# Performance work log

Measured on AMD Instinct MI355X. Metric: run time of the kernel, lower is better.

The kernel has to match this reference:

```python
import jax, jax.numpy as jnp
import numpy as np

B, C, H, W = 2, 192, 64, 64
HEADS, KS = 6, 7
HD = C // HEADS


def setup_inputs() -> dict:
    key = jax.random.key(0)
    ks = jax.random.split(key, 6)
    s = 0.02
    return {
        "x": jax.random.normal(ks[0], (B, C, H, W), jnp.float32),
        "W_qkv1": jax.random.normal(ks[1], (3 * C, C, 1, 1), jnp.float32) * s,
        "b_qkv1": jnp.zeros((3 * C,), jnp.float32),
        "W_qkv2": jax.random.normal(ks[2], (3 * C, 1, 3, 3), jnp.float32) * s,  # depthwise
        "b_qkv2": jnp.zeros((3 * C,), jnp.float32),
        "temperature": jnp.ones((HEADS, 1, 1, 1), jnp.float32),
        "rpb": jax.random.normal(ks[3], (HEADS, 2 * KS - 1, 2 * KS - 1), jnp.float32) * s,
        "W_proj": jax.random.normal(ks[4], (C, C, 1, 1), jnp.float32) * s,
        "b_proj": jnp.zeros((C,), jnp.float32),
    }


def _conv(x, w, b, pad, groups=1):
    y = jax.lax.conv_general_dilated(
        x, w, (1, 1), pad,
        dimension_numbers=("NCHW", "OIHW", "NCHW"),
        feature_group_count=groups)
    return y + b[None, :, None, None]


def _l2norm(t, eps=1e-12):
    n = jnp.sqrt(jnp.sum(t * t, axis=-1, keepdims=True))
    return t / jnp.maximum(n, eps)


def _nbr_idx(L, K):
    # NATTEN shifted-window neighborhood (dilation=1): window start clamped to image.
    start = jnp.clip(jnp.arange(L) - K // 2, 0, L - K)
    idx = start[:, None] + jnp.arange(K)[None, :]        # [L,K] absolute neighbor index
    rel = idx - jnp.arange(L)[:, None] + (K - 1)         # [L,K] rpb table index
    return idx, rel


def _forward(x, W_qkv1, b_qkv1, W_qkv2, b_qkv2, temperature, rpb, W_proj, b_proj):
    Bq, Cq, Hh, Ww = x.shape
    heads = rpb.shape[0]
    K = (rpb.shape[1] + 1) // 2
    hd = Cq // heads
    qkv = _conv(_conv(x, W_qkv1, b_qkv1, "VALID"), W_qkv2, b_qkv2, "SAME", groups=3 * Cq)
    qkv = qkv.reshape(Bq, 3, heads, hd, Hh, Ww).transpose(1, 0, 2, 4, 5, 3)  # [3,B,h,H,W,d]
    q, k, v = qkv[0], qkv[1], qkv[2]
    q = _l2norm(q)
    k = _l2norm(k)
    idx_i, rel_i = _nbr_idx(Hh, K)
    idx_j, rel_j = _nbr_idx(Ww, K)
    ii = idx_i[:, None, :, None]  # [H,1,K,1]
    jj = idx_j[None, :, None, :]  # [1,W,1,K] -> broadcast [H,W,K,K]
    k_nb = k[:, :, ii, jj, :]     # [B,h,H,W,K,K,d]
    attn = jnp.einsum("bhijd,bhijkld->bhijkl", q, k_nb)
    bias = rpb[:, rel_i[:, None, :, None], rel_j[None, :, None, :]]  # [h,H,W,K,K]
    attn = (attn + bias[None]) * temperature.reshape(1, heads, 1, 1, 1, 1)
    attn = jax.nn.softmax(attn.reshape(Bq, heads, Hh, Ww, K * K), axis=-1)
    v_nb = v[:, :, ii, jj, :].reshape(Bq, heads, Hh, Ww, K * K, hd)
    out = jnp.einsum("bhijk,bhijkd->bhijd", attn, v_nb)
    out = out.transpose(0, 1, 4, 2, 3).reshape(Bq, Cq, Hh, Ww)
    return _conv(out, W_proj, b_proj, "VALID")


def reference(x, W_qkv1, b_qkv1, W_qkv2, b_qkv2, temperature, rpb, W_proj, b_proj):
    return _forward(x, W_qkv1, b_qkv1, W_qkv2, b_qkv2, temperature, rpb, W_proj, b_proj)
```

## Files before the change

### kernel.cpp

```cpp
#include <hip/hip_runtime.h>
#include <math.h>

#define HW 4096

typedef __attribute__((ext_vector_type(8))) short short8;
typedef __attribute__((ext_vector_type(8))) _Float16 half8;
typedef __attribute__((ext_vector_type(4))) float floatx4;

__device__ inline float bflo(unsigned u) { return __uint_as_float(u << 16); }
__device__ inline float bfhi(unsigned u) { return __uint_as_float(u & 0xffff0000u); }
__device__ inline unsigned short f2bf(float x) {
    unsigned u = __float_as_uint(x);
    return (unsigned short)((u + 0x7fffu + ((u >> 16) & 1u)) >> 16);
}
__device__ inline unsigned f2bf2(float lo, float hi) {
    unsigned a = __float_as_uint(lo), b = __float_as_uint(hi);
    a = (a + 0x7fffu + ((a >> 16) & 1u)) >> 16;
    b = (b + 0x7fffu + ((b >> 16) & 1u)) & 0xffff0000u;
    return a | b;
}
__device__ inline unsigned short f2h(float x) {
    _Float16 h = (_Float16)x;
    return __builtin_bit_cast(unsigned short, h);
}

__device__ inline void stage_halo(unsigned short* raw, const unsigned short* pl,
                                  int t, int npx, int gi0, int gj0)
{
    if (t < npx) {
        int ri = t >> 4, rj = t & 15;
        int gi = gi0 + ri, gj = gj0 + rj;
        uint4 v0 = {0u,0u,0u,0u}, v1 = v0, v2 = v0, v3 = v0;
        if ((unsigned)gi < 64u && (unsigned)gj < 64u) {
            const uint4* src = (const uint4*)(pl + (((gi << 6) + gj) << 5));
            v0 = src[0]; v1 = src[1]; v2 = src[2]; v3 = src[3];
        }
        uint4* d = (uint4*)&raw[t * 32];
        d[0] = v0; d[1] = v1; d[2] = v2; d[3] = v3;
    }
}


__global__ __launch_bounds__(256) void k_gq(const float* __restrict__ x,
    const float* __restrict__ W1, const float* __restrict__ b1,
    unsigned short* __restrict__ qkv)
{
    __shared__ __align__(16) unsigned short As[64 * 200];
    __shared__ __align__(16) unsigned short Bs[64 * 200];
    const int t = threadIdx.x;
    const int m0 = blockIdx.x * 64;
    const int n0 = blockIdx.y * 64;
    const int w = t >> 6, lane = t & 63;
    const int b = m0 >> 12, px0 = m0 & 4095;
    {
        const float* xb = x + ((size_t)(b * 192) << 12) + px0 + lane;
        const int cb = w * 48;
        #pragma unroll
        for (int r4 = 0; r4 < 12; ++r4) {
            float v0 = xb[(size_t)(cb + r4 * 4 + 0) << 12];
            float v1 = xb[(size_t)(cb + r4 * 4 + 1) << 12];
            float v2 = xb[(size_t)(cb + r4 * 4 + 2) << 12];
            float v3 = xb[(size_t)(cb + r4 * 4 + 3) << 12];
            *(uint2*)&As[lane * 200 + cb + r4 * 4] =
                make_uint2(f2bf2(v0, v1), f2bf2(v2, v3));
        }
    }
    #pragma unroll
    for (int pass = 0; pass < 12; ++pass) {
        int idx = pass * 256 + t;
        int row = idx / 48, ch = idx - row * 48;
        float4 wv = *(const float4*)&W1[(size_t)(n0 + row) * 192 + ch * 4];
        *(uint2*)&Bs[row * 200 + ch * 4] =
            make_uint2(f2bf2(wv.x, wv.y), f2bf2(wv.z, wv.w));
    }
    __syncthreads();
    const int lm = lane & 15, lq = lane >> 4;
    floatx4 acc[4] = {};
    #pragma unroll
    for (int ks = 0; ks < 6; ++ks) {
        short8 bf = *(const short8*)&Bs[(w * 16 + lm) * 200 + ks * 32 + lq * 8];
        #pragma unroll
        for (int mt = 0; mt < 4; ++mt) {
            short8 af = *(const short8*)&As[(mt * 16 + lm) * 200 + ks * 32 + lq * 8];
            acc[mt] = __builtin_amdgcn_mfma_f32_16x16x32_bf16(af, bf, acc[mt], 0, 0, 0);
        }
    }
    __syncthreads();
    const float bias = b1[n0 + w * 16 + lm];
    #pragma unroll
    for (int mt = 0; mt < 4; ++mt)
        #pragma unroll
        for (int r = 0; r < 4; ++r)
            As[(mt * 16 + lq * 4 + r) * 72 + w * 16 + lm] = f2bf(acc[mt][r] + bias);
    __syncthreads();
    #pragma unroll
    for (int pass = 0; pass < 2; ++pass) {
        int idx = pass * 256 + t;
        int m = idx >> 3, n8 = idx & 7;
        uint4 val = *(const uint4*)&As[m * 72 + n8 * 8];
        int oc = n0 + n8 * 8;
        int g = oc >> 5, d = oc & 31;
        *(uint4*)&qkv[((((size_t)(b * 18 + g) << 12) + px0 + m) << 5) + d] = val;
    }
}

__global__ __launch_bounds__(256) void k_attn(const unsigned short* __restrict__ qkv,
    const float* __restrict__ W2, const float* __restrict__ b2,
    const float* __restrict__ temp, const float* __restrict__ rpb,
    unsigned short* __restrict__ attnO)
{
    __shared__ __align__(16) char lds[49088];
    unsigned short* Ks  = (unsigned short*)lds;
    unsigned short* Ps  = (unsigned short*)lds;
    unsigned short* raw = (unsigned short*)(lds + 16640);
    unsigned short* Vts = (unsigned short*)(lds + 29696);
    float* rpbs = (float*)(lds + 44544);
    float* dwW  = (float*)(lds + 45248);
    float* dwB  = (float*)(lds + 48704);

    const int t = threadIdx.x;
    const int head = blockIdx.y, b = blockIdx.z;
    const int ti = blockIdx.x >> 3, tj = blockIdx.x & 7;
    const int i0 = ti * 8, j0 = tj * 8;
    const int r0 = min(max(i0 - 3, 0), 50), c0 = min(max(j0 - 3, 0), 50);
    const unsigned short* qpl = qkv + ((size_t)(b * 18 + head) << 17);
    const unsigned short* kpl = qkv + ((size_t)(b * 18 + 6 + head) << 17);
    const unsigned short* vpl = qkv + ((size_t)(b * 18 + 12 + head) << 17);

    for (int idx = t; idx < 864; idx += 256) {
        int plane = idx / 288, rem = idx - plane * 288;
        dwW[idx] = W2[(plane * 192 + head * 32 + (rem & 31)) * 9 + (rem >> 5)];
    }
    if (t < 96) dwB[t] = b2[(t >> 5) * 192 + head * 32 + (t & 31)];
    if (t < 169) rpbs[t] = rpb[head * 169 + t];
    for (int idx = t; idx < 448; idx += 256) {
        int row = (idx * 2341) >> 15;
        int c = idx - row * 14;
        ((unsigned*)(Vts + row * 232))[98 + c] = 0u;
    }

    for (int h = 0; h < 2; ++h) {
        stage_halo(raw, kpl, t, 144, r0 - 1 + h * 7, c0 - 1);
        __syncthreads();
        for (int s = 0; s < 2; ++s) {
            int task = s * 256 + t;
            if (task < 392) {
                int px = task >> 2, oct = task & 3;
                int rl = (px * 2341) >> 15, cc = px - rl * 14;
                float a[8];
                #pragma unroll
                for (int e = 0; e < 8; ++e) a[e] = dwB[32 + oct * 8 + e];
                #pragma unroll
                for (int tap = 0; tap < 9; ++tap) {
                    uint4 u = *(const uint4*)&raw[((rl + tap / 3) * 16 + cc + tap % 3) * 32 + oct * 8];
                    const float* wt = &dwW[(9 + tap) * 32 + oct * 8];
                    unsigned uu[4] = {u.x, u.y, u.z, u.w};
                    #pragma unroll
                    for (int e = 0; e < 4; ++e) {
                        a[e * 2]     = fmaf(bflo(uu[e]), wt[e * 2],     a[e * 2]);
                        a[e * 2 + 1] = fmaf(bfhi(uu[e]), wt[e * 2 + 1], a[e * 2 + 1]);
                    }
                }
                float ss = 0.f;
                #pragma unroll
                for (int e = 0; e < 8; ++e) ss = fmaf(a[e], a[e], ss);
                ss += __shfl_xor(ss, 1);
                ss += __shfl_xor(ss, 2);
                float rinv = 1.0f / fmaxf(sqrtf(ss), 1e-12f);
                int pxk = (h * 7 + rl) * 14 + cc;
                uint4 p;
                p.x = f2bf2(a[0] * rinv, a[1] * rinv);
                p.y = f2bf2(a[2] * rinv, a[3] * rinv);
                p.z = f2bf2(a[4] * rinv, a[5] * rinv);
                p.w = f2bf2(a[6] * rinv, a[7] * rinv);
                *(uint4*)&Ks[pxk * 40 + oct * 8] = p;
            }
        }
        __syncthreads();
    }

    for (int h = 0; h < 2; ++h) {
        stage_halo(raw, vpl, t, 144, r0 - 1 + h * 7, c0 - 1);
        __syncthreads();
        for (int s = 0; s < 2; ++s) {
            int task = s * 256 + t;
            if (task < 392) {
                int px = task >> 2, oct = task & 3;
                int rl = (px * 2341) >> 15, cc = px - rl * 14;
                float a[8];
                #pragma unroll
                for (int e = 0; e < 8; ++e) a[e] = dwB[64 + oct * 8 + e];
                #pragma unroll
                for (int tap = 0; tap < 9; ++tap) {
                    uint4 u = *(const uint4*)&raw[((rl + tap / 3) * 16 + cc + tap % 3) * 32 + oct * 8];
                    const float* wt = &dwW[(18 + tap) * 32 + oct * 8];
                    unsigned uu[4] = {u.x, u.y, u.z, u.w};
                    #pragma unroll
                    for (int e = 0; e < 4; ++e) {
                        a[e * 2]     = fmaf(bflo(uu[e]), wt[e * 2],     a[e * 2]);
                        a[e * 2 + 1] = fmaf(bfhi(uu[e]), wt[e * 2 + 1], a[e * 2 + 1]);
                    }
                }
                int pxk = (h * 7 + rl) * 14 + cc;
                #pragma unroll
                for (int e = 0; e < 8; ++e)
                    Vts[(oct * 8 + e) * 232 + pxk] = f2h(a[e]);
            }
        }
        __syncthreads();
    }

    stage_halo(raw, qpl, t, 160, i0 - 1, c0 - 1);
    __syncthreads();
    const int w = t >> 6, lane = t & 63;
    const int lm = lane & 15, lq = lane >> 4;
    const int px = w * 16 + lm;
    const int i = i0 + (px >> 3), j = j0 + (px & 7);
    const int qrow = px >> 3, qcol = (px & 7) + (j0 - c0);
    float qf[8];
    #pragma unroll
    for (int e = 0; e < 8; ++e) qf[e] = dwB[lq * 8 + e];
    #pragma unroll
    for (int tap = 0; tap < 9; ++tap) {
        uint4 u = *(const uint4*)&raw[((qrow + tap / 3) * 16 + qcol + tap % 3) * 32 + lq * 8];
        const float* wt = &dwW[tap * 32 + lq * 8];
        unsigned uu[4] = {u.x, u.y, u.z, u.w};
        #pragma unroll
        for (int e = 0; e < 4; ++e) {
            qf[e * 2]     = fmaf(bflo(uu[e]), wt[e * 2],     qf[e * 2]);
            qf[e * 2 + 1] = fmaf(bfhi(uu[e]), wt[e * 2 + 1], qf[e * 2 + 1]);
        }
    }
    float qs = 0.f;
    #pragma unroll
    for (int e = 0; e < 8; ++e) qs = fmaf(qf[e], qf[e], qs);
    qs += __shfl_xor(qs, 16);
    qs += __shfl_xor(qs, 32);
    float qinv = 1.0f / fmaxf(sqrtf(qs), 1e-12f);
    short8 bq;
    #pragma unroll
    for (int e = 0; e < 8; ++e) bq[e] = (short)f2bf(qf[e] * qinv);
    __syncthreads();

    floatx4 acc[13];
    #pragma unroll
    for (int mt = 0; mt < 13; ++mt) {
        short8 ak = *(const short8*)&Ks[(mt * 16 + lm) * 40 + lq * 8];
        floatx4 z = {0.f, 0.f, 0.f, 0.f};
        acc[mt] = __builtin_amdgcn_mfma_f32_16x16x32_bf16(ak, bq, z, 0, 0, 0);
    }
    __syncthreads();

    const int si = min(max(i - 3, 0), 57), sj = min(max(j - 3, 0), 57);
    const int vloi = si - r0, vloj = sj - c0;
    const int oi = r0 - i + 6, oj = c0 - j + 6;
    const float th = temp[head];
    float mx = -1e30f;
    #pragma unroll
    for (int mt = 0; mt < 13; ++mt) {
        int nb0 = mt * 16 + lq * 4;
        int rh0 = (nb0 * 2341) >> 15;
        int ch0 = nb0 - rh0 * 14;
        #pragma unroll
        for (int r = 0; r < 4; ++r) {
            int ch = ch0 + r, rh = rh0;
            if (ch >= 14) { ch -= 14; rh += 1; }
            int bidx = (rh + oi) * 13 + (ch + oj);
            float bias = rpbs[max(0, min(168, bidx))];
            bool valid = ((unsigned)(rh - vloi) <= 6u) && ((unsigned)(ch - vloj) <= 6u);
            float s = (acc[mt][r] + bias) * th;
            s = valid ? s : -1e30f;
            acc[mt][r] = s;
            mx = fmaxf(mx, s);
        }
    }
    mx = fmaxf(mx, __shfl_xor(mx, 16));
    mx = fmaxf(mx, __shfl_xor(mx, 32));
    float ssum = 0.f;
    #pragma unroll
    for (int mt = 0; mt < 13; ++mt)
        #pragma unroll
        for (int r = 0; r < 4; ++r) {
            float e = __expf(acc[mt][r] - mx);
            acc[mt][r] = e;
            ssum += e;
        }
    ssum += __shfl_xor(ssum, 16);
    ssum += __shfl_xor(ssum, 32);
    const float rs = 1.0f / ssum;

    if (lane < 32) {
        uint4 z4 = {0u, 0u, 0u, 0u};
        *(uint4*)&Ps[(w * 16 + (lane >> 1)) * 232 + 208 + (lane & 1) * 8] = z4;
    }
    #pragma unroll
    for (int mt = 0; mt < 13; ++mt) {
        unsigned lo = (unsigned)f2h(acc[mt][0] * rs) | ((unsigned)f2h(acc[mt][1] * rs) << 16);
        unsigned hi = (unsigned)f2h(acc[mt][2] * rs) | ((unsigned)f2h(acc[mt][3] * rs) << 16);
        *(uint2*)&Ps[px * 232 + mt * 16 + lq * 4] = make_uint2(lo, hi);
    }
    __syncthreads();

    floatx4 oacc[2] = {};
    #pragma unroll
    for (int ks = 0; ks < 7; ++ks) {
        half8 ap = *(const half8*)&Ps[(w * 16 + lm) * 232 + ks * 32 + lq * 8];
        #pragma unroll
        for (int n2 = 0; n2 < 2; ++n2) {
            half8 bv = *(const half8*)&Vts[(n2 * 16 + lm) * 232 + ks * 32 + lq * 8];
            oacc[n2] = __builtin_amdgcn_mfma_f32_16x16x32_f16(ap, bv, oacc[n2], 0, 0, 0);
        }
    }
    #pragma unroll
    for (int n2 = 0; n2 < 2; ++n2)
        #pragma unroll
        for (int r = 0; r < 4; ++r) {
            int p2 = w * 16 + lq * 4 + r;
            int i2 = i0 + (p2 >> 3), j2 = j0 + (p2 & 7);
            attnO[((size_t)((b << 12) + (i2 << 6) + j2)) * 192 + head * 32 + n2 * 16 + lm]
                = f2bf(oacc[n2][r]);
        }
}

__global__ __launch_bounds__(256) void k_gp(const unsigned short* __restrict__ Ain,
    const float* __restrict__ Wp, const float* __restrict__ bp,
    float* __restrict__ out)
{
    __shared__ __align__(16) unsigned short As[64 * 200];
    __shared__ __align__(16) unsigned short Bs[64 * 200];
    const int t = threadIdx.x;
    const int m0 = blockIdx.x * 64;
    const int n0 = blockIdx.y * 64;
    #pragma unroll
    for (int pass = 0; pass < 6; ++pass) {
        int idx = pass * 256 + t;
        int m = idx / 24, c16 = idx % 24;
        *(uint4*)&As[m * 200 + c16 * 8] = *(const uint4*)&Ain[(size_t)(m0 + m) * 192 + c16 * 8];
    }
    #pragma unroll
    for (int pass = 0; pass < 12; ++pass) {
        int idx = pass * 256 + t;
        int row = idx / 48, ch = idx - row * 48;
        float4 wv = *(const float4*)&Wp[(size_t)(n0 + row) * 192 + ch * 4];
        *(uint2*)&Bs[row * 200 + ch * 4] =
            make_uint2(f2bf2(wv.x, wv.y), f2bf2(wv.z, wv.w));
    }
    __syncthreads();
    const int w = t >> 6, lane = t & 63;
    const int lm = lane & 15, lq = lane >> 4;
    floatx4 acc[4] = {};
    #pragma unroll
    for (int ks = 0; ks < 6; ++ks) {
        short8 bf = *(const short8*)&Bs[(w * 16 + lm) * 200 + ks * 32 + lq * 8];
        #pragma unroll
        for (int mt = 0; mt < 4; ++mt) {
            short8 af = *(const short8*)&As[(mt * 16 + lm) * 200 + ks * 32 + lq * 8];
            acc[mt] = __builtin_amdgcn_mfma_f32_16x16x32_bf16(af, bf, acc[mt], 0, 0, 0);
        }
    }
    __syncthreads();
    float* fs = (float*)As;
    const float bias = bp[n0 + w * 16 + lm];
    #pragma unroll
    for (int mt = 0; mt < 4; ++mt)
        #pragma unroll
        for (int r = 0; r < 4; ++r)
            fs[(w * 16 + lm) * 68 + mt * 16 + lq * 4 + r] = acc[mt][r] + bias;
    __syncthreads();
    const int b = m0 >> 12, px0 = m0 & 4095;
    #pragma unroll
    for (int pass = 0; pass < 4; ++pass) {
        int idx = pass * 256 + t;
        int n = idx >> 4, m4 = idx & 15;
        float4 val = *(const float4*)&fs[n * 68 + m4 * 4];
        *(float4*)&out[((size_t)(b * 192 + n0 + n) << 12) + px0 + m4 * 4] = val;
    }
}

extern "C" void kernel_launch(void* const* d_in, const int* in_sizes, int n_in,
                              void* d_out, int out_size, void* d_ws, size_t ws_size,
                              hipStream_t stream) {
    const float* x    = (const float*)d_in[0];
    const float* W1   = (const float*)d_in[1];
    const float* b1   = (const float*)d_in[2];
    const float* W2   = (const float*)d_in[3];
    const float* b2   = (const float*)d_in[4];
    const float* temp = (const float*)d_in[5];
    const float* rpb  = (const float*)d_in[6];
    const float* Wp   = (const float*)d_in[7];
    const float* bp   = (const float*)d_in[8];
    float* out = (float*)d_out;

    char* ws = (char*)d_ws;
    unsigned short* qkv1b = (unsigned short*)(ws);
    unsigned short* attnO = (unsigned short*)(ws + 9437184);

    k_gq  <<<dim3(128, 9), 256, 0, stream>>>(x, W1, b1, qkv1b);
    k_attn<<<dim3(64, 6, 2), 256, 0, stream>>>(qkv1b, W2, b2, temp, rpb, attnO);
    k_gp  <<<dim3(128, 3), 256, 0, stream>>>(attnO, Wp, bp, out);
}
```

Measured before the change: 115.7 us.

## Fuse three kernels into one persistent kernel with grid-wide barriers

Merges the QKV GEMM, neighborhood attention and projection GEMM kernels into a single persistent kernel of 512 blocks. The blocks loop over tiles and are separated by atomic-counter grid barriers. The goal is to remove kernel launch gaps and the tail effects between stages. In exchange it adds a memset, spin-wait barriers, and a dependence on all 512 blocks being co-resident (2 per CU at 51 KB of LDS), which could deadlock if occupancy is lower. The later stages also leave some blocks idle.

```diff
diff --git a/kernel.cpp b/kernel.cpp
--- a/kernel.cpp
+++ b/kernel.cpp
@@ -1,7 +1,5 @@
 #include <hip/hip_runtime.h>
 #include <math.h>
-
-#define HW 4096
 
 typedef __attribute__((ext_vector_type(8))) short short8;
 typedef __attribute__((ext_vector_type(8))) _Float16 half8;
@@ -24,8 +22,8 @@
     return __builtin_bit_cast(unsigned short, h);
 }
 
-__device__ inline void stage_halo(unsigned short* raw, const unsigned short* pl,
-                                  int t, int npx, int gi0, int gj0)
+__device__ __forceinline__ void stage_halo(unsigned short* raw, const unsigned short* pl,
+                                           int t, int npx, int gi0, int gj0)
 {
     if (t < npx) {
         int ri = t >> 4, rj = t & 15;
@@ -40,16 +38,29 @@
     }
 }
 
-
-__global__ __launch_bounds__(256) void k_gq(const float* __restrict__ x,
-    const float* __restrict__ W1, const float* __restrict__ b1,
-    unsigned short* __restrict__ qkv)
-{
-    __shared__ __align__(16) unsigned short As[64 * 200];
-    __shared__ __align__(16) unsigned short Bs[64 * 200];
+__device__ __forceinline__ void grid_barrier(unsigned* bar, unsigned target)
+{
+    __syncthreads();
+    if (threadIdx.x == 0) {
+        __threadfence();
+        __hip_atomic_fetch_add(bar, 1u, __ATOMIC_RELEASE, __HIP_MEMORY_SCOPE_AGENT);
+        while (__hip_atomic_load(bar, __ATOMIC_ACQUIRE, __HIP_MEMORY_SCOPE_AGENT) < target) {
+            __builtin_amdgcn_s_sleep(8);
+        }
+        __threadfence();
+    }
+    __syncthreads();
+}
+
+
+__device__ void gq_tile(char* smem, int tile, const float* x, const float* W1,
+                        const float* b1, unsigned short* qkv)
+{
+    unsigned short* As = (unsigned short*)smem;
+    unsigned short* Bs = (unsigned short*)(smem + 25600);
     const int t = threadIdx.x;
-    const int m0 = blockIdx.x * 64;
-    const int n0 = blockIdx.y * 64;
+    const int m0 = (tile & 127) * 64;
+    const int n0 = (tile >> 7) * 64;
     const int w = t >> 6, lane = t & 63;
     const int b = m0 >> 12, px0 = m0 & 4095;
     {
@@ -102,14 +113,14 @@
         int g = oc >> 5, d = oc & 31;
         *(uint4*)&qkv[((((size_t)(b * 18 + g) << 12) + px0 + m) << 5) + d] = val;
     }
-}
-
-__global__ __launch_bounds__(256) void k_attn(const unsigned short* __restrict__ qkv,
-    const float* __restrict__ W2, const float* __restrict__ b2,
-    const float* __restrict__ temp, const float* __restrict__ rpb,
-    unsigned short* __restrict__ attnO)
-{
-    __shared__ __align__(16) char lds[49088];
+    __syncthreads();
+}
+
+__device__ void attn_tile(char* smem, int tile, const unsigned short* qkv,
+    const float* W2, const float* b2, const float* temp, const float* rpb,
+    unsigned short* attnO)
+{
+    char* lds = smem;
     unsigned short* Ks  = (unsigned short*)lds;
     unsigned short* Ps  = (unsigned short*)lds;
     unsigned short* raw = (unsigned short*)(lds + 16640);
@@ -119,8 +130,10 @@
     float* dwB  = (float*)(lds + 48704);
 
     const int t = threadIdx.x;
-    const int head = blockIdx.y, b = blockIdx.z;
-    const int ti = blockIdx.x >> 3, tj = blockIdx.x & 7;
+    const int hb = tile >> 6;
+    const int b = hb / 6, head = hb - b * 6;
+    const int bx = tile & 63;
+    const int ti = bx >> 3, tj = bx & 7;
     const int i0 = ti * 8, j0 = tj * 8;
     const int r0 = min(max(i0 - 3, 0), 50), c0 = min(max(j0 - 3, 0), 50);
     const unsigned short* qpl = qkv + ((size_t)(b * 18 + head) << 17);
@@ -320,17 +333,17 @@
             attnO[((size_t)((b << 12) + (i2 << 6) + j2)) * 192 + head * 32 + n2 * 16 + lm]
                 = f2bf(oacc[n2][r]);
         }
-}
-
-__global__ __launch_bounds__(256) void k_gp(const unsigned short* __restrict__ Ain,
-    const float* __restrict__ Wp, const float* __restrict__ bp,
-    float* __restrict__ out)
-{
-    __shared__ __align__(16) unsigned short As[64 * 200];
-    __shared__ __align__(16) unsigned short Bs[64 * 200];
+    __syncthreads();
+}
+
+__device__ void gp_tile(char* smem, int tile, const unsigned short* Ain,
+    const float* Wp, const float* bp, float* out)
+{
+    unsigned short* As = (unsigned short*)smem;
+    unsigned short* Bs = (unsigned short*)(smem + 25600);
     const int t = threadIdx.x;
-    const int m0 = blockIdx.x * 64;
-    const int n0 = blockIdx.y * 64;
+    const int m0 = (tile & 127) * 64;
+    const int n0 = (tile >> 7) * 64;
     #pragma unroll
     for (int pass = 0; pass < 6; ++pass) {
         int idx = pass * 256 + t;
@@ -375,6 +388,31 @@
         float4 val = *(const float4*)&fs[n * 68 + m4 * 4];
         *(float4*)&out[((size_t)(b * 192 + n0 + n) << 12) + px0 + m4 * 4] = val;
     }
+    __syncthreads();
+}
+
+__global__ __launch_bounds__(256, 2) void k_fused(
+    const float* __restrict__ x, const float* __restrict__ W1, const float* __restrict__ b1,
+    const float* __restrict__ W2, const float* __restrict__ b2,
+    const float* __restrict__ temp, const float* __restrict__ rpb,
+    const float* __restrict__ Wp, const float* __restrict__ bp,
+    unsigned short* __restrict__ qkv1b, unsigned short* __restrict__ attnO,
+    float* __restrict__ out, unsigned* bar)
+{
+    __shared__ __align__(16) char smem[51200];
+
+    for (int tile = blockIdx.x; tile < 1152; tile += 512)
+        gq_tile(smem, tile, x, W1, b1, qkv1b);
+
+    grid_barrier(bar, 512);
+
+    for (int tile = blockIdx.x; tile < 768; tile += 512)
+        attn_tile(smem, tile, qkv1b, W2, b2, temp, rpb, attnO);
+
+    grid_barrier(bar, 1024);
+
+    for (int tile = blockIdx.x; tile < 384; tile += 512)
+        gp_tile(smem, tile, attnO, Wp, bp, out);
 }
 
 extern "C" void kernel_launch(void* const* d_in, const int* in_sizes, int n_in,
@@ -394,8 +432,10 @@
     char* ws = (char*)d_ws;
     unsigned short* qkv1b = (unsigned short*)(ws);
     unsigned short* attnO = (unsigned short*)(ws + 9437184);
-
-    k_gq  <<<dim3(128, 9), 256, 0, stream>>>(x, W1, b1, qkv1b);
-    k_attn<<<dim3(64, 6, 2), 256, 0, stream>>>(qkv1b, W2, b2, temp, rpb, attnO);
-    k_gp  <<<dim3(128, 3), 256, 0, stream>>>(attnO, Wp, bp, out);
-}
+    unsigned* bar         = (unsigned*)(ws + 16777216);
+
+    hipMemsetAsync(bar, 0, 64, stream);
+
+    k_fused<<<dim3(512), dim3(256), 0, stream>>>(
+        x, W1, b1, W2, b2, temp, rpb, Wp, bp, qkv1b, attnO, out, bar);
+}
```

Result: slower. 272.9 us (+135.8%).
